# Performance work log

Measured on AMD Instinct MI355X. Metric: run time of the kernel, lower is better.

The kernel has to match this reference:

```python
import jax, jax.numpy as jnp
import numpy as np

B, S, D = 2, 4096, 768
H = 12
HD = D // H  # 64


def setup_inputs() -> dict:
    key = jax.random.key(0)
    ks = jax.random.split(key, 6)
    scale = 0.02
    return {
        "x": jax.random.normal(ks[0], (B, S, D), dtype=jnp.float32),
        "w_query": jax.random.normal(ks[1], (D, D), dtype=jnp.float32) * scale,
        "w_key": jax.random.normal(ks[2], (D, D), dtype=jnp.float32) * scale,
        "w_value": jax.random.normal(ks[3], (D, D), dtype=jnp.float32) * scale,
        "w_out": jax.random.normal(ks[4], (D, D), dtype=jnp.float32) * scale,
        "b_out": jax.random.normal(ks[5], (D,), dtype=jnp.float32) * scale,
    }


def reference(x, w_query, w_key, w_value, w_out, b_out):
    b, s, d = x.shape
    # Linear(in, out) applies x @ W.T; weights here stored as [out, in]-equivalent
    # square matrices, so use x @ W.T for parity with torch semantics.
    q = (x @ w_query.T).reshape(b, s, H, HD).transpose(0, 2, 1, 3)  # [b,h,s,hd]
    k = (x @ w_key.T).reshape(b, s, H, HD).transpose(0, 2, 1, 3)
    v = (x @ w_value.T).reshape(b, s, H, HD).transpose(0, 2, 1, 3)

    scores = jnp.einsum("bhqd,bhkd->bhqk", q, k)  # [b,h,s,s]
    causal = jnp.triu(jnp.ones((s, s), dtype=bool), k=1)
    scores = jnp.where(causal, -jnp.inf, scores)
    # original scales AFTER masking: softmax(masked / sqrt(head_dim))
    att = jax.nn.softmax(scores / jnp.sqrt(jnp.float32(HD)), axis=-1)
    # dropout p=0.0 (eval) -> identity
    ctx = jnp.einsum("bhqk,bhkd->bhqd", att, v)  # [b,h,s,hd]
    ctx = ctx.transpose(0, 2, 1, 3).reshape(b, s, d)
    return ctx @ w_out.T + b_out
```

## Files before the change

kernel.cpp:

```cpp
#include <hip/hip_runtime.h>
#include <stdint.h>

typedef unsigned short u16;
typedef __attribute__((ext_vector_type(8))) short bf16x8;
typedef __attribute__((ext_vector_type(4))) float f32x4;

#define MFMA(a,b,c) __builtin_amdgcn_mfma_f32_16x16x32_bf16((a),(b),(c),0,0,0)

static constexpr int S  = 4096;
static constexpr int D  = 768;
static constexpr int H  = 12;
static constexpr int HD = 64;

__device__ __forceinline__ u16 f2b(float f){
  union { float f; unsigned u; } v; v.f = f;
  unsigned r = (v.u + 0x7fffu + ((v.u >> 16) & 1u)) >> 16;
  return (u16)r;
}

__device__ __forceinline__ unsigned pack_bf16_trunc(float a, float b){
  return __builtin_amdgcn_perm(__float_as_uint(b), __float_as_uint(a), 0x07060302u);
}

__device__ __forceinline__ void cp16(const u16* g, u16* l){
  __builtin_amdgcn_global_load_lds(
      (const __attribute__((address_space(1))) unsigned int*)g,
      (__attribute__((address_space(3))) unsigned int*)l, 16, 0, 0);
}

__device__ __forceinline__ bf16x8 quad_transpose(unsigned M0, unsigned M1,
                                                 unsigned M2, unsigned M3){
  auto r0 = __builtin_amdgcn_permlane32_swap(M0, M2, false, false);
  auto r1 = __builtin_amdgcn_permlane32_swap(M1, M3, false, false);
  auto s0 = __builtin_amdgcn_permlane16_swap(r0[0], r0[1], false, false);
  auto s1 = __builtin_amdgcn_permlane16_swap(r1[0], r1[1], false, false);
  union { unsigned u[4]; bf16x8 v; } r;
  r.u[0] = s0[0];
  r.u[1] = s1[0];
  r.u[2] = s0[1];
  r.u[3] = s1[1];
  return r.v;
}

static constexpr int NX4 = (2 * S * D) / 4;
static constexpr int NW4 = (D * D) / 4;
__global__ void castall(const float* __restrict__ x,  const float* __restrict__ wq,
                        const float* __restrict__ wk, const float* __restrict__ wv,
                        const float* __restrict__ wo,
                        u16* __restrict__ xb,  u16* __restrict__ wqb,
                        u16* __restrict__ wkb, u16* __restrict__ wvb,
                        u16* __restrict__ wob){
  int i = blockIdx.x * 256 + threadIdx.x;
  const float* s; u16* d; int off;
  if (i < NX4) { s = x; d = xb; off = i; }
  else {
    int j = i - NX4; int wsel = j / NW4; off = j - wsel * NW4;
    if (wsel >= 4) return;
    s = (wsel == 0) ? wq : (wsel == 1) ? wk : (wsel == 2) ? wv : wo;
    d = (wsel == 0) ? wqb : (wsel == 1) ? wkb : (wsel == 2) ? wvb : wob;
  }
  float4 v = ((const float4*)s)[off];
  uint2 o;
  o.x = (unsigned)f2b(v.x) | ((unsigned)f2b(v.y) << 16);
  o.y = (unsigned)f2b(v.z) | ((unsigned)f2b(v.w) << 16);
  ((uint2*)d)[off] = o;
}

__global__ __launch_bounds__(256, 2) void qkv_gemm(
    const u16* __restrict__ xb, const u16* __restrict__ wq, const u16* __restrict__ wk,
    const u16* __restrict__ wv, u16* __restrict__ Qb, u16* __restrict__ Kb, u16* __restrict__ Vt)
{
  __shared__ __align__(16) u16 As[128 * 64];
  __shared__ __align__(16) u16 Bs[128 * 64];
  const int t = threadIdx.x;
  const int mblk = blockIdx.x, nblk = blockIdx.y, z = blockIdx.z;
  const u16* W = (z == 0) ? wq : (z == 1) ? wk : wv;
  const int w = t >> 6, lane = t & 63, quad = lane >> 4, l16 = lane & 15;
  const int wr = w >> 1, wc = w & 1;
  const int l7 = l16 & 7;

  f32x4 acc[4][4];
  #pragma unroll
  for (int i = 0; i < 4; i++)
    #pragma unroll
    for (int j = 0; j < 4; j++) acc[i][j] = (f32x4){0.f, 0.f, 0.f, 0.f};

  int srow[4], schk[4];
  #pragma unroll
  for (int i = 0; i < 4; i++) {
    int s = i * 256 + t;
    srow[i] = s >> 3;
    schk[i] = (s & 7) ^ (srow[i] & 7);
  }
  const u16* gA = xb + (size_t)(mblk * 128) * D;
  const u16* gB = W  + (size_t)(nblk * 128) * D;

  for (int k0 = 0; k0 < D; k0 += 64) {
    __syncthreads();
    #pragma unroll
    for (int i = 0; i < 4; i++) {
      int s = i * 256 + t;
      cp16(gA + (size_t)srow[i] * D + k0 + schk[i] * 8, As + s * 8);
      cp16(gB + (size_t)srow[i] * D + k0 + schk[i] * 8, Bs + s * 8);
    }
    __syncthreads();
    #pragma unroll
    for (int j = 0; j < 2; j++) {
      bf16x8 af[4], bfr[4];
      #pragma unroll
      for (int mt = 0; mt < 4; mt++)
        af[mt]  = *(const bf16x8*)(As + (wr * 64 + mt * 16 + l16) * 64 + ((j * 4 + quad) ^ l7) * 8);
      #pragma unroll
      for (int nt = 0; nt < 4; nt++)
        bfr[nt] = *(const bf16x8*)(Bs + (wc * 64 + nt * 16 + l16) * 64 + ((j * 4 + quad) ^ l7) * 8);
      #pragma unroll
      for (int mt = 0; mt < 4; mt++)
        #pragma unroll
        for (int nt = 0; nt < 4; nt++)
          acc[mt][nt] = MFMA(af[mt], bfr[nt], acc[mt][nt]);
    }
  }

  const float qscale = 0.18033688011112042f;
  #pragma unroll
  for (int mt = 0; mt < 4; mt++) {
    int m0 = mblk * 128 + wr * 64 + mt * 16 + quad * 4;
    #pragma unroll
    for (int nt = 0; nt < 4; nt++) {
      int n = nblk * 128 + wc * 64 + nt * 16 + l16;
      int h = n >> 6, hd = n & 63;
      if (z == 2) {
        int b = m0 >> 12, s0 = m0 & 4095;
        u16* p = Vt + (((size_t)(b * H + h) * HD + hd)) * S + s0;
        uint2 pk;
        pk.x = (unsigned)f2b(acc[mt][nt][0]) | ((unsigned)f2b(acc[mt][nt][1]) << 16);
        pk.y = (unsigned)f2b(acc[mt][nt][2]) | ((unsigned)f2b(acc[mt][nt][3]) << 16);
        *(uint2*)p = pk;
      } else {
        u16* dst = (z == 0) ? Qb : Kb;
        float sc = (z == 0) ? qscale : 1.0f;
        #pragma unroll
        for (int r = 0; r < 4; r++) {
          int m = m0 + r; int b = m >> 12, s = m & 4095;
          dst[((size_t)(b * H + h) * S + s) * HD + hd] = f2b(acc[mt][nt][r] * sc);
        }
      }
    }
  }
}

__global__ __launch_bounds__(256, 2) void attn(
    const u16* __restrict__ Qb, const u16* __restrict__ Kb,
    const u16* __restrict__ Vt, u16* __restrict__ ctx)
{
  __shared__ __align__(16) u16 Ks[2][64 * 64];
  __shared__ __align__(16) u16 Vts[2][64 * 64];
  __shared__ float Lbuf[2][2][16];
  const int t = threadIdx.x, w = t >> 6, lane = t & 63, quad = lane >> 4, l16 = lane & 15;
  const int l7 = l16 & 7;
  const int wq = w >> 1, wk = w & 1;

  const int p       = (int)blockIdx.x;
  const int bh      = p % 24;
  const int qtile64 = 63 - p / 24;
  const int q0 = qtile64 * 64;
  const int nt = qtile64 + 1;

  const u16* Qh = Qb + (size_t)bh * S * HD;
  const u16* Kh = Kb + (size_t)bh * S * HD;
  const u16* Vh = Vt + (size_t)bh * S * HD;
  const int b = bh / H, h = bh % H;

  bf16x8 qf[2][2];
  #pragma unroll
  for (int qt = 0; qt < 2; qt++)
    #pragma unroll
    for (int ksh = 0; ksh < 2; ksh++)
      qf[qt][ksh] = *(const bf16x8*)(Qh + (size_t)(q0 + wq * 32 + qt * 16 + l16) * HD + ksh * 32 + quad * 8);
  asm volatile("s_waitcnt vmcnt(0)" ::: "memory");

  f32x4 ao[2][4];
  #pragma unroll
  for (int qt = 0; qt < 2; qt++)
    #pragma unroll
    for (int co = 0; co < 4; co++) ao[qt][co] = (f32x4){0.f, 0.f, 0.f, 0.f};
  float lsum[2] = {0.f, 0.f};

  const int r0 = t >> 3;
  const int c0 = (t & 7) ^ (r0 & 7);

  auto stage = [&](int kv, int d){
    cp16(Kh + (size_t)(kv + r0)      * HD + c0 * 8, &Ks[d][0] + t * 8);
    cp16(Kh + (size_t)(kv + r0 + 32) * HD + c0 * 8, &Ks[d][0] + (t + 256) * 8);
    cp16(Vh + (size_t)r0 * S        + kv + c0 * 8, &Vts[d][0] + t * 8);
    cp16(Vh + (size_t)(r0 + 32) * S + kv + c0 * 8, &Vts[d][0] + (t + 256) * 8);
  };

  stage(0, 0);

  for (int it = 0; it < nt; ++it) {
    const int cur = it & 1;
    const bool diag = (it == nt - 1);
    if (!diag) stage((it + 1) * 64, cur ^ 1);
    if (!diag) asm volatile("s_waitcnt vmcnt(4)\ns_barrier" ::: "memory");
    else       asm volatile("s_waitcnt vmcnt(0)\ns_barrier" ::: "memory");

    const bool skipall = diag && (wk == 1) && (wq == 0);
    const bool mdiag   = diag && (wk == wq);

    if (!skipall) {
      const u16* Kc = &Ks[cur][0];
      const u16* Vc = &Vts[cur][0];
      unsigned pA[2][2], pB[2][2];
      #pragma unroll
      for (int ktL = 0; ktL < 2; ktL++) {
        const int krw = wk * 32 + ktL * 16 + l16;
        bf16x8 kf0 = *(const bf16x8*)(Kc + krw * 64 + ((0 + quad) ^ l7) * 8);
        bf16x8 kf1 = *(const bf16x8*)(Kc + krw * 64 + ((4 + quad) ^ l7) * 8);
        #pragma unroll
        for (int qt = 0; qt < 2; qt++) {
          f32x4 s0 = (f32x4){0.f, 0.f, 0.f, 0.f};
          __builtin_amdgcn_s_setprio(1);
          s0 = MFMA(kf0, qf[qt][0], s0);
          s0 = MFMA(kf1, qf[qt][1], s0);
          __builtin_amdgcn_s_setprio(0);
          if (mdiag) {
            const int qoff = (qt - ktL) * 16 + l16;
            #pragma unroll
            for (int r = 0; r < 4; r++)
              s0[r] = (quad * 4 + r > qoff) ? -1e30f : s0[r];
          }
          float p0 = __builtin_amdgcn_exp2f(s0[0]);
          float p1 = __builtin_amdgcn_exp2f(s0[1]);
          float p2 = __builtin_amdgcn_exp2f(s0[2]);
          float p3 = __builtin_amdgcn_exp2f(s0[3]);
          lsum[qt] += (p0 + p1) + (p2 + p3);
          pA[qt][ktL] = pack_bf16_trunc(p0, p1);
          pB[qt][ktL] = pack_bf16_trunc(p2, p3);
        }
      }
      bf16x8 pf[2];
      #pragma unroll
      for (int qt = 0; qt < 2; qt++)
        pf[qt] = quad_transpose(pA[qt][0], pB[qt][0], pA[qt][1], pB[qt][1]);
      __builtin_amdgcn_s_setprio(1);
      #pragma unroll
      for (int co = 0; co < 4; co++) {
        const int vrw = co * 16 + l16;
        bf16x8 vf = *(const bf16x8*)(Vc + vrw * 64 + ((wk * 4 + quad) ^ (vrw & 7)) * 8);
        #pragma unroll
        for (int qt = 0; qt < 2; qt++)
          ao[qt][co] = MFMA(vf, pf[qt], ao[qt][co]);
      }
      __builtin_amdgcn_s_setprio(0);
    }
    asm volatile("s_barrier" ::: "memory");
  }

  #pragma unroll
  for (int qt = 0; qt < 2; qt++) {
    float v = lsum[qt];
    v += __shfl_xor(v, 16, 64);
    v += __shfl_xor(v, 32, 64);
    lsum[qt] = v;
  }

  float* red = wq ? (float*)&Vts[0][0] : (float*)&Ks[0][0];
  if (wk == 1) {
    #pragma unroll
    for (int qt = 0; qt < 2; qt++)
      #pragma unroll
      for (int co = 0; co < 4; co++)
        *(f32x4*)(red + ((qt * 4 + co) * 64 + lane) * 4) = ao[qt][co];
    if (lane < 16) {
      #pragma unroll
      for (int qt = 0; qt < 2; qt++) Lbuf[wq][qt][lane] = lsum[qt];
    }
  }
  __syncthreads();
  if (wk == 0) {
    #pragma unroll
    for (int qt = 0; qt < 2; qt++) {
      float tot = lsum[qt] + Lbuf[wq][qt][l16];
      float inv = 1.0f / tot;
      int token = b * S + q0 + wq * 32 + qt * 16 + l16;
      #pragma unroll
      for (int co = 0; co < 4; co++) {
        f32x4 pr = *(const f32x4*)(red + ((qt * 4 + co) * 64 + lane) * 4);
        f32x4 sv = ao[qt][co] + pr;
        uint2 pk;
        pk.x = (unsigned)f2b(sv[0] * inv) | ((unsigned)f2b(sv[1] * inv) << 16);
        pk.y = (unsigned)f2b(sv[2] * inv) | ((unsigned)f2b(sv[3] * inv) << 16);
        *(uint2*)(ctx + (size_t)token * D + h * HD + co * 16 + quad * 4) = pk;
      }
    }
  }
}

__global__ __launch_bounds__(256, 2) void out_gemm(
    const u16* __restrict__ ctx, const u16* __restrict__ wo,
    const float* __restrict__ bias, float* __restrict__ out)
{
  __shared__ __align__(16) u16 As[128 * 64];
  __shared__ __align__(16) u16 Bs[128 * 64];
  const int t = threadIdx.x;
  const int mblk = blockIdx.x, nblk = blockIdx.y;
  const int w = t >> 6, lane = t & 63, quad = lane >> 4, l16 = lane & 15;
  const int wr = w >> 1, wc = w & 1;
  const int l7 = l16 & 7;

  f32x4 acc[4][4];
  #pragma unroll
  for (int i = 0; i < 4; i++)
    #pragma unroll
    for (int j = 0; j < 4; j++) acc[i][j] = (f32x4){0.f, 0.f, 0.f, 0.f};

  int srow[4], schk[4];
  #pragma unroll
  for (int i = 0; i < 4; i++) {
    int s = i * 256 + t;
    srow[i] = s >> 3;
    schk[i] = (s & 7) ^ (srow[i] & 7);
  }
  const u16* gA = ctx + (size_t)(mblk * 128) * D;
  const u16* gB = wo  + (size_t)(nblk * 128) * D;

  for (int k0 = 0; k0 < D; k0 += 64) {
    __syncthreads();
    #pragma unroll
    for (int i = 0; i < 4; i++) {
      int s = i * 256 + t;
      cp16(gA + (size_t)srow[i] * D + k0 + schk[i] * 8, As + s * 8);
      cp16(gB + (size_t)srow[i] * D + k0 + schk[i] * 8, Bs + s * 8);
    }
    __syncthreads();
    #pragma unroll
    for (int j = 0; j < 2; j++) {
      bf16x8 af[4], bfr[4];
      #pragma unroll
      for (int mt = 0; mt < 4; mt++)
        af[mt]  = *(const bf16x8*)(As + (wr * 64 + mt * 16 + l16) * 64 + ((j * 4 + quad) ^ l7) * 8);
      #pragma unroll
      for (int nt = 0; nt < 4; nt++)
        bfr[nt] = *(const bf16x8*)(Bs + (wc * 64 + nt * 16 + l16) * 64 + ((j * 4 + quad) ^ l7) * 8);
      #pragma unroll
      for (int mt = 0; mt < 4; mt++)
        #pragma unroll
        for (int nt = 0; nt < 4; nt++)
          acc[mt][nt] = MFMA(af[mt], bfr[nt], acc[mt][nt]);
    }
  }

  #pragma unroll
  for (int mt = 0; mt < 4; mt++) {
    int m0 = mblk * 128 + wr * 64 + mt * 16 + quad * 4;
    #pragma unroll
    for (int nt = 0; nt < 4; nt++) {
      int n = nblk * 128 + wc * 64 + nt * 16 + l16;
      float bv = bias[n];
      #pragma unroll
      for (int r = 0; r < 4; r++)
        out[(size_t)(m0 + r) * D + n] = acc[mt][nt][r] + bv;
    }
  }
}

extern "C" void kernel_launch(void* const* d_in, const int* in_sizes, int n_in,
                              void* d_out, int out_size, void* d_ws, size_t ws_size,
                              hipStream_t stream) {
  const float* x    = (const float*)d_in[0];
  const float* wq   = (const float*)d_in[1];
  const float* wk   = (const float*)d_in[2];
  const float* wv   = (const float*)d_in[3];
  const float* wo   = (const float*)d_in[4];
  const float* bo   = (const float*)d_in[5];
  float* out = (float*)d_out;

  u16* ws = (u16*)d_ws;
  const size_t NX = (size_t)2 * S * D;
  const size_t NW = (size_t)D * D;
  u16* xb  = ws;
  u16* wqb = ws + NX;
  u16* wkb = wqb + NW;
  u16* wvb = wkb + NW;
  u16* wob = wvb + NW;
  u16* Qb  = wob + NW;
  u16* Kb  = Qb + NX;
  u16* Vt  = Kb + NX;
  u16* ctx = xb;

  const int total4 = NX4 + 4 * NW4;
  castall<<<(total4 + 255) / 256, 256, 0, stream>>>(x, wq, wk, wv, wo, xb, wqb, wkb, wvb, wob);

  qkv_gemm<<<dim3(64, 6, 3), 256, 0, stream>>>(xb, wqb, wkb, wvb, Qb, Kb, Vt);
  attn<<<dim3(1536), 256, 0, stream>>>(Qb, Kb, Vt, ctx);
  out_gemm<<<dim3(64, 6), 256, 0, stream>>>(ctx, wob, bo, out);
}
```

Baseline: 211.8 us.

## Double-buffer LDS tiles with K=32 steps in QKV and output GEMMs

Measured after the change: 223.2 us. 5.4% more time.

```diff
diff --git a/kernel.cpp b/kernel.cpp
--- a/kernel.cpp
+++ b/kernel.cpp
@@ -66,18 +66,17 @@
   ((uint2*)d)[off] = o;
 }
 
-__global__ __launch_bounds__(256, 2) void qkv_gemm(
+__global__ __launch_bounds__(256, 4) void qkv_gemm(
     const u16* __restrict__ xb, const u16* __restrict__ wq, const u16* __restrict__ wk,
     const u16* __restrict__ wv, u16* __restrict__ Qb, u16* __restrict__ Kb, u16* __restrict__ Vt)
 {
-  __shared__ __align__(16) u16 As[128 * 64];
-  __shared__ __align__(16) u16 Bs[128 * 64];
+  __shared__ __align__(16) u16 As[2][128 * 32];
+  __shared__ __align__(16) u16 Bs[2][128 * 32];
   const int t = threadIdx.x;
   const int mblk = blockIdx.x, nblk = blockIdx.y, z = blockIdx.z;
   const u16* W = (z == 0) ? wq : (z == 1) ? wk : wv;
   const int w = t >> 6, lane = t & 63, quad = lane >> 4, l16 = lane & 15;
   const int wr = w >> 1, wc = w & 1;
-  const int l7 = l16 & 7;
 
   f32x4 acc[4][4];
   #pragma unroll
@@ -85,40 +84,44 @@
     #pragma unroll
     for (int j = 0; j < 4; j++) acc[i][j] = (f32x4){0.f, 0.f, 0.f, 0.f};
 
-  int srow[4], schk[4];
-  #pragma unroll
-  for (int i = 0; i < 4; i++) {
-    int s = i * 256 + t;
-    srow[i] = s >> 3;
-    schk[i] = (s & 7) ^ (srow[i] & 7);
-  }
+  const int r0 = t >> 2;
+  const int gc = (t & 3) ^ ((r0 >> 1) & 3);
   const u16* gA = xb + (size_t)(mblk * 128) * D;
   const u16* gB = W  + (size_t)(nblk * 128) * D;
 
-  for (int k0 = 0; k0 < D; k0 += 64) {
-    __syncthreads();
-    #pragma unroll
-    for (int i = 0; i < 4; i++) {
-      int s = i * 256 + t;
-      cp16(gA + (size_t)srow[i] * D + k0 + schk[i] * 8, As + s * 8);
-      cp16(gB + (size_t)srow[i] * D + k0 + schk[i] * 8, Bs + s * 8);
-    }
-    __syncthreads();
-    #pragma unroll
-    for (int j = 0; j < 2; j++) {
-      bf16x8 af[4], bfr[4];
-      #pragma unroll
-      for (int mt = 0; mt < 4; mt++)
-        af[mt]  = *(const bf16x8*)(As + (wr * 64 + mt * 16 + l16) * 64 + ((j * 4 + quad) ^ l7) * 8);
+  auto stage = [&](int it, int d){
+    const int k0 = it * 32;
+    cp16(gA + (size_t)r0 * D        + k0 + gc * 8, &As[d][0] + t * 8);
+    cp16(gA + (size_t)(r0 + 64) * D + k0 + gc * 8, &As[d][0] + (t + 256) * 8);
+    cp16(gB + (size_t)r0 * D        + k0 + gc * 8, &Bs[d][0] + t * 8);
+    cp16(gB + (size_t)(r0 + 64) * D + k0 + gc * 8, &Bs[d][0] + (t + 256) * 8);
+  };
+
+  stage(0, 0);
+  const int fA = (quad ^ ((l16 >> 1) & 3)) * 8;
+
+  for (int it = 0; it < 24; ++it) {
+    const int cur = it & 1;
+    const bool last = (it == 23);
+    if (!last) {
+      stage(it + 1, cur ^ 1);
+      asm volatile("s_waitcnt vmcnt(4)\ns_barrier" ::: "memory");
+    } else {
+      asm volatile("s_waitcnt vmcnt(0)\ns_barrier" ::: "memory");
+    }
+    bf16x8 af[4], bfr[4];
+    #pragma unroll
+    for (int mt = 0; mt < 4; mt++)
+      af[mt]  = *(const bf16x8*)(&As[cur][0] + (wr * 64 + mt * 16 + l16) * 32 + fA);
+    #pragma unroll
+    for (int nt = 0; nt < 4; nt++)
+      bfr[nt] = *(const bf16x8*)(&Bs[cur][0] + (wc * 64 + nt * 16 + l16) * 32 + fA);
+    #pragma unroll
+    for (int mt = 0; mt < 4; mt++)
       #pragma unroll
       for (int nt = 0; nt < 4; nt++)
-        bfr[nt] = *(const bf16x8*)(Bs + (wc * 64 + nt * 16 + l16) * 64 + ((j * 4 + quad) ^ l7) * 8);
-      #pragma unroll
-      for (int mt = 0; mt < 4; mt++)
-        #pragma unroll
-        for (int nt = 0; nt < 4; nt++)
-          acc[mt][nt] = MFMA(af[mt], bfr[nt], acc[mt][nt]);
-    }
+        acc[mt][nt] = MFMA(af[mt], bfr[nt], acc[mt][nt]);
+    asm volatile("s_barrier" ::: "memory");
   }
 
   const float qscale = 0.18033688011112042f;
@@ -301,13 +304,12 @@
     const u16* __restrict__ ctx, const u16* __restrict__ wo,
     const float* __restrict__ bias, float* __restrict__ out)
 {
-  __shared__ __align__(16) u16 As[128 * 64];
-  __shared__ __align__(16) u16 Bs[128 * 64];
+  __shared__ __align__(16) u16 As[2][128 * 32];
+  __shared__ __align__(16) u16 Bs[2][128 * 32];
   const int t = threadIdx.x;
   const int mblk = blockIdx.x, nblk = blockIdx.y;
   const int w = t >> 6, lane = t & 63, quad = lane >> 4, l16 = lane & 15;
   const int wr = w >> 1, wc = w & 1;
-  const int l7 = l16 & 7;
 
   f32x4 acc[4][4];
   #pragma unroll
@@ -315,40 +317,44 @@
     #pragma unroll
     for (int j = 0; j < 4; j++) acc[i][j] = (f32x4){0.f, 0.f, 0.f, 0.f};
 
-  int srow[4], schk[4];
-  #pragma unroll
-  for (int i = 0; i < 4; i++) {
-    int s = i * 256 + t;
-    srow[i] = s >> 3;
-    schk[i] = (s & 7) ^ (srow[i] & 7);
-  }
+  const int r0 = t >> 2;
+  const int gc = (t & 3) ^ ((r0 >> 1) & 3);
   const u16* gA = ctx + (size_t)(mblk * 128) * D;
   const u16* gB = wo  + (size_t)(nblk * 128) * D;
 
-  for (int k0 = 0; k0 < D; k0 += 64) {
-    __syncthreads();
-    #pragma unroll
-    for (int i = 0; i < 4; i++) {
-      int s = i * 256 + t;
-      cp16(gA + (size_t)srow[i] * D + k0 + schk[i] * 8, As + s * 8);
-      cp16(gB + (size_t)srow[i] * D + k0 + schk[i] * 8, Bs + s * 8);
-    }
-    __syncthreads();
-    #pragma unroll
-    for (int j = 0; j < 2; j++) {
-      bf16x8 af[4], bfr[4];
-      #pragma unroll
-      for (int mt = 0; mt < 4; mt++)
-        af[mt]  = *(const bf16x8*)(As + (wr * 64 + mt * 16 + l16) * 64 + ((j * 4 + quad) ^ l7) * 8);
+  auto stage = [&](int it, int d){
+    const int k0 = it * 32;
+    cp16(gA + (size_t)r0 * D        + k0 + gc * 8, &As[d][0] + t * 8);
+    cp16(gA + (size_t)(r0 + 64) * D + k0 + gc * 8, &As[d][0] + (t + 256) * 8);
+    cp16(gB + (size_t)r0 * D        + k0 + gc * 8, &Bs[d][0] + t * 8);
+    cp16(gB + (size_t)(r0 + 64) * D + k0 + gc * 8, &Bs[d][0] + (t + 256) * 8);
+  };
+
+  stage(0, 0);
+  const int fA = (quad ^ ((l16 >> 1) & 3)) * 8;
+
+  for (int it = 0; it < 24; ++it) {
+    const int cur = it & 1;
+    const bool last = (it == 23);
+    if (!last) {
+      stage(it + 1, cur ^ 1);
+      asm volatile("s_waitcnt vmcnt(4)\ns_barrier" ::: "memory");
+    } else {
+      asm volatile("s_waitcnt vmcnt(0)\ns_barrier" ::: "memory");
+    }
+    bf16x8 af[4], bfr[4];
+    #pragma unroll
+    for (int mt = 0; mt < 4; mt++)
+      af[mt]  = *(const bf16x8*)(&As[cur][0] + (wr * 64 + mt * 16 + l16) * 32 + fA);
+    #pragma unroll
+    for (int nt = 0; nt < 4; nt++)
+      bfr[nt] = *(const bf16x8*)(&Bs[cur][0] + (wc * 64 + nt * 16 + l16) * 32 + fA);
+    #pragma unroll
+    for (int mt = 0; mt < 4; mt++)
       #pragma unroll
       for (int nt = 0; nt < 4; nt++)
-        bfr[nt] = *(const bf16x8*)(Bs + (wc * 64 + nt * 16 + l16) * 64 + ((j * 4 + quad) ^ l7) * 8);
-      #pragma unroll
-      for (int mt = 0; mt < 4; mt++)
-        #pragma unroll
-        for (int nt = 0; nt < 4; nt++)
-          acc[mt][nt] = MFMA(af[mt], bfr[nt], acc[mt][nt]);
-    }
+        acc[mt][nt] = MFMA(af[mt], bfr[nt], acc[mt][nt]);
+    asm volatile("s_barrier" ::: "memory");
   }
 
   #pragma unroll
```

## Drop K/V double buffering and raise attention kernel occupancy target

Applied to the files above, without the earlier changes.

After: 645.4 us. 205% more time.

```diff
diff --git a/kernel.cpp b/kernel.cpp
--- a/kernel.cpp
+++ b/kernel.cpp
@@ -149,12 +149,12 @@
   }
 }
 
-__global__ __launch_bounds__(256, 2) void attn(
+__global__ __launch_bounds__(256, 8) void attn(
     const u16* __restrict__ Qb, const u16* __restrict__ Kb,
     const u16* __restrict__ Vt, u16* __restrict__ ctx)
 {
-  __shared__ __align__(16) u16 Ks[2][64 * 64];
-  __shared__ __align__(16) u16 Vts[2][64 * 64];
+  __shared__ __align__(16) u16 Ks[64 * 64];
+  __shared__ __align__(16) u16 Vts[64 * 64];
   __shared__ float Lbuf[2][2][16];
   const int t = threadIdx.x, w = t >> 6, lane = t & 63, quad = lane >> 4, l16 = lane & 15;
   const int l7 = l16 & 7;
@@ -177,7 +177,6 @@
     #pragma unroll
     for (int ksh = 0; ksh < 2; ksh++)
       qf[qt][ksh] = *(const bf16x8*)(Qh + (size_t)(q0 + wq * 32 + qt * 16 + l16) * HD + ksh * 32 + quad * 8);
-  asm volatile("s_waitcnt vmcnt(0)" ::: "memory");
 
   f32x4 ao[2][4];
   #pragma unroll
@@ -189,34 +188,26 @@
   const int r0 = t >> 3;
   const int c0 = (t & 7) ^ (r0 & 7);
 
-  auto stage = [&](int kv, int d){
-    cp16(Kh + (size_t)(kv + r0)      * HD + c0 * 8, &Ks[d][0] + t * 8);
-    cp16(Kh + (size_t)(kv + r0 + 32) * HD + c0 * 8, &Ks[d][0] + (t + 256) * 8);
-    cp16(Vh + (size_t)r0 * S        + kv + c0 * 8, &Vts[d][0] + t * 8);
-    cp16(Vh + (size_t)(r0 + 32) * S + kv + c0 * 8, &Vts[d][0] + (t + 256) * 8);
-  };
-
-  stage(0, 0);
-
   for (int it = 0; it < nt; ++it) {
-    const int cur = it & 1;
-    const bool diag = (it == nt - 1);
-    if (!diag) stage((it + 1) * 64, cur ^ 1);
-    if (!diag) asm volatile("s_waitcnt vmcnt(4)\ns_barrier" ::: "memory");
-    else       asm volatile("s_waitcnt vmcnt(0)\ns_barrier" ::: "memory");
-
+    const int kv0 = it * 64;
+    const bool diag    = (it == nt - 1);
     const bool skipall = diag && (wk == 1) && (wq == 0);
     const bool mdiag   = diag && (wk == wq);
 
+    __syncthreads();
+    cp16(Kh + (size_t)(kv0 + r0)      * HD + c0 * 8, Ks + t * 8);
+    cp16(Kh + (size_t)(kv0 + r0 + 32) * HD + c0 * 8, Ks + (t + 256) * 8);
+    cp16(Vh + (size_t)r0 * S        + kv0 + c0 * 8, Vts + t * 8);
+    cp16(Vh + (size_t)(r0 + 32) * S + kv0 + c0 * 8, Vts + (t + 256) * 8);
+    __syncthreads();
+
     if (!skipall) {
-      const u16* Kc = &Ks[cur][0];
-      const u16* Vc = &Vts[cur][0];
       unsigned pA[2][2], pB[2][2];
       #pragma unroll
       for (int ktL = 0; ktL < 2; ktL++) {
         const int krw = wk * 32 + ktL * 16 + l16;
-        bf16x8 kf0 = *(const bf16x8*)(Kc + krw * 64 + ((0 + quad) ^ l7) * 8);
-        bf16x8 kf1 = *(const bf16x8*)(Kc + krw * 64 + ((4 + quad) ^ l7) * 8);
+        bf16x8 kf0 = *(const bf16x8*)(Ks + krw * 64 + ((0 + quad) ^ l7) * 8);
+        bf16x8 kf1 = *(const bf16x8*)(Ks + krw * 64 + ((4 + quad) ^ l7) * 8);
         #pragma unroll
         for (int qt = 0; qt < 2; qt++) {
           f32x4 s0 = (f32x4){0.f, 0.f, 0.f, 0.f};
@@ -247,14 +238,13 @@
       #pragma unroll
       for (int co = 0; co < 4; co++) {
         const int vrw = co * 16 + l16;
-        bf16x8 vf = *(const bf16x8*)(Vc + vrw * 64 + ((wk * 4 + quad) ^ (vrw & 7)) * 8);
+        bf16x8 vf = *(const bf16x8*)(Vts + vrw * 64 + ((wk * 4 + quad) ^ (vrw & 7)) * 8);
         #pragma unroll
         for (int qt = 0; qt < 2; qt++)
           ao[qt][co] = MFMA(vf, pf[qt], ao[qt][co]);
       }
       __builtin_amdgcn_s_setprio(0);
     }
-    asm volatile("s_barrier" ::: "memory");
   }
 
   #pragma unroll
@@ -265,7 +255,8 @@
     lsum[qt] = v;
   }
 
-  float* red = wq ? (float*)&Vts[0][0] : (float*)&Ks[0][0];
+  __syncthreads();
+  float* red = wq ? (float*)Vts : (float*)Ks;
   if (wk == 1) {
     #pragma unroll
     for (int qt = 0; qt < 2; qt++)
```
